# Optimization experiments

Measured on AMD Instinct MI355X. Metric: run time of the kernel, lower is better.

The kernel has to match this reference:

```python
import jax, jax.numpy as jnp
import numpy as np
from jax import lax

B, C, H, W = 32, 256, 56, 56

def _conv(x, w, stride, groups=1, pad='VALID'):
    return lax.conv_general_dilated(x, w, (stride, stride), pad,
                                    feature_group_count=groups,
                                    dimension_numbers=('NCHW', 'OIHW', 'NCHW'))

def _ln(x, g, b, eps=1e-5):
    mu = jnp.mean(x, -1, keepdims=True)
    var = jnp.mean((x - mu) ** 2, -1, keepdims=True)
    return (x - mu) * lax.rsqrt(var + eps) * g + b

def setup_inputs() -> dict:
    key = jax.random.key(0)
    ks = jax.random.split(key, 16)
    s = 0.02
    Ch = C // 2
    d = {}
    d['x'] = jax.random.normal(ks[0], (B, C, H, W), jnp.float32)
    d['Wq'] = jax.random.normal(ks[1], (C, C), jnp.float32) * s;  d['bq'] = jnp.zeros((C,), jnp.float32)
    d['Wk'] = jax.random.normal(ks[2], (C, C), jnp.float32) * s;  d['bk'] = jnp.zeros((C,), jnp.float32)
    d['Wv'] = jax.random.normal(ks[3], (C, C), jnp.float32) * s;  d['bv'] = jnp.zeros((C,), jnp.float32)
    d['sr1_w'] = jax.random.normal(ks[4], (C, C, 8, 8), jnp.float32) * s; d['sr1_b'] = jnp.zeros((C,), jnp.float32)
    d['ln1_g'] = jnp.ones((C,), jnp.float32); d['ln1_b'] = jnp.zeros((C,), jnp.float32)
    d['sr2_w'] = jax.random.normal(ks[5], (C, C, 4, 4), jnp.float32) * s; d['sr2_b'] = jnp.zeros((C,), jnp.float32)
    d['ln2_g'] = jnp.ones((C,), jnp.float32); d['ln2_b'] = jnp.zeros((C,), jnp.float32)
    d['Wkv1'] = jax.random.normal(ks[6], (C, C), jnp.float32) * s; d['bkv1'] = jnp.zeros((C,), jnp.float32)
    d['Wkv2'] = jax.random.normal(ks[7], (C, C), jnp.float32) * s; d['bkv2'] = jnp.zeros((C,), jnp.float32)
    d['lc1_w'] = jax.random.normal(ks[8], (Ch, 1, 3, 3), jnp.float32) * s; d['lc1_b'] = jnp.zeros((Ch,), jnp.float32)
    d['lc2_w'] = jax.random.normal(ks[9], (Ch, 1, 3, 3), jnp.float32) * s; d['lc2_b'] = jnp.zeros((Ch,), jnp.float32)
    d['rp_w'] = jax.random.normal(ks[10], (C, C), jnp.float32) * s;  d['rp_b'] = jnp.zeros((C,), jnp.float32)
    d['rp12_w'] = jax.random.normal(ks[11], (C, C), jnp.float32) * s; d['rp12_b'] = jnp.zeros((C,), jnp.float32)
    d['dw_w'] = jax.random.normal(ks[12], (C, 2), jnp.float32) * 0.5  # Conv3d (2,1,1) depthwise, no bias
    return d

def reference(x, Wq, bq, Wk, bk, Wv, bv, sr1_w, sr1_b, ln1_g, ln1_b,
              sr2_w, sr2_b, ln2_g, ln2_b, Wkv1, bkv1, Wkv2, bkv2,
              lc1_w, lc1_b, lc2_w, lc2_b, rp_w, rp_b, rp12_w, rp12_b, dw_w):
    Bx, Cc, h, w = x.shape
    N = h * w
    Ch = Cc // 2
    xt = x.reshape(Bx, Cc, N).transpose(0, 2, 1)                 # [B,N,C]
    q = jax.nn.softmax(xt @ Wq + bq, axis=-1)                    # softmax over channels
    q1, q2 = q[..., :Ch], q[..., Ch:]

    # spatial-reduction branches (conv -> LN -> GELU)
    x1 = _conv(x, sr1_w, 8) + sr1_b[:, None, None]               # [B,C,7,7]
    x1 = jax.nn.gelu(_ln(x1.reshape(Bx, Cc, -1).transpose(0, 2, 1), ln1_g, ln1_b), approximate=False)
    x2 = _conv(x, sr2_w, 4) + sr2_b[:, None, None]               # [B,C,14,14]
    x2 = jax.nn.gelu(_ln(x2.reshape(Bx, Cc, -1).transpose(0, 2, 1), ln2_g, ln2_b), approximate=False)

    def branch(xr, Wkv, bkv, lc_w, lc_b, qh, hh):
        kv = (xr @ Wkv + bkv).reshape(Bx, -1, 2, Ch)
        k = jax.nn.softmax(kv[:, :, 0], axis=1)                  # softmax over reduced tokens
        v = kv[:, :, 1]
        vsp = v.transpose(0, 2, 1).reshape(Bx, Ch, hh, hh)
        v = v + (_conv(vsp, lc_w, 1, groups=Ch, pad='SAME') + lc_b[:, None, None]).reshape(Bx, Ch, -1).transpose(0, 2, 1)
        ctx = jnp.einsum('bnk,bnv->bkv', k, v)                   # [B,Ch,Ch]
        return jnp.einsum('bnk,bkv->bnv', qh, ctx)               # [B,N,Ch]

    a1 = branch(x1, Wkv1, bkv1, lc1_w, lc1_b, q1, 7)
    a2 = branch(x2, Wkv2, bkv2, lc2_w, lc2_b, q2, 14)
    eff2 = jnp.concatenate([a1, a2], axis=-1)                    # [B,N,C]
    eff2 = jnp.einsum('bni,oi->bon', eff2, rp12_w).reshape(Bx, Cc, h, w) + rp12_b[None, :, None, None]

    # global efficient-attention branch
    keys = jax.nn.softmax(xt @ Wk + bk, axis=1)                  # softmax over tokens
    values = xt @ Wv + bv
    ctx = jnp.einsum('bnk,bnv->bkv', keys, values)               # [B,C,C]
    att = jnp.einsum('bnk,bkv->bnv', q, ctx)                     # [B,N,C]
    eff = jnp.einsum('bni,oi->bon', att, rp_w).reshape(Bx, Cc, h, w) + rp_b[None, :, None, None]

    # Conv3d (2,1,1) depthwise merge over the two branches
    out = eff * dw_w[:, 0][None, :, None, None] + eff2 * dw_w[:, 1][None, :, None, None]
    return out
```

## Files before the change

### kernel.cpp

```cpp
#include <hip/hip_runtime.h>
#include <hip/hip_bf16.h>
#include <math.h>

#define B_ 32
#define H_ 56
#define W_ 56
#define N_ 3136
#define NT_ 100352

typedef short short8 __attribute__((ext_vector_type(8)));
typedef float f32x4 __attribute__((ext_vector_type(4)));

__device__ __forceinline__ unsigned short f2b(float f){
  union { float f; unsigned u; } v; v.f = f;
  return (unsigned short)((v.u + 0x7FFFu + ((v.u>>16)&1u)) >> 16);
}

#define LDSW(row, bo) ((unsigned)((row)*128 + ((bo) ^ (((row)&7)<<4))))

__device__ __forceinline__ short8 ldfrag(const char* base, int row, int kk){
  return *(const short8*)(base + LDSW(row, kk*2));
}
__device__ __forceinline__ f32x4 mfma16(short8 a, short8 b, f32x4 c){
  return __builtin_amdgcn_mfma_f32_16x16x32_bf16(a, b, c, 0, 0, 0);
}

__global__ void prep_kernel(const float* __restrict__ Wq, const float* __restrict__ Wk,
                            const float* __restrict__ Wv, const float* __restrict__ Wkv1,
                            const float* __restrict__ Wkv2, const float* __restrict__ sr1w,
                            const float* __restrict__ sr2w, const float* __restrict__ rpw,
                            const float* __restrict__ rpb, const float* __restrict__ rp12w,
                            const float* __restrict__ rp12b, const float* __restrict__ dww,
                            unsigned short* WqT, unsigned short* WkT, unsigned short* WvT,
                            unsigned short* Wkv1T, unsigned short* Wkv2T,
                            unsigned short* srw1, unsigned short* srw2,
                            unsigned short* Acomb, float* bias_out)
{
  int idx = blockIdx.x*256 + threadIdx.x;
  const int total = 5*65536 + 4194304 + 1048576 + 131072 + 256;
  for (int i = idx; i < total; i += gridDim.x*256) {
    int j = i;
    if (j < 5*65536) {
      int w = j >> 16, e = j & 65535;
      int o = e >> 8, c = e & 255;
      const float* src = (w==0)?Wq:(w==1)?Wk:(w==2)?Wv:(w==3)?Wkv1:Wkv2;
      unsigned short* dst = (w==0)?WqT:(w==1)?WkT:(w==2)?WvT:(w==3)?Wkv1T:Wkv2T;
      dst[o*256+c] = f2b(src[c*256+o]);
      continue;
    }
    j -= 5*65536;
    if (j < 4194304) {
      int o = j >> 14, rem = j & 16383, pos = rem >> 8, c = rem & 255;
      srw1[j] = f2b(sr1w[o*16384 + c*64 + pos]);
      continue;
    }
    j -= 4194304;
    if (j < 1048576) {
      int o = j >> 12, rem = j & 4095, pos = rem >> 8, c = rem & 255;
      srw2[j] = f2b(sr2w[o*4096 + c*16 + pos]);
      continue;
    }
    j -= 1048576;
    if (j < 131072) {
      int o = j >> 9, i2 = j & 511;
      float v = (i2 < 256) ? dww[o*2+0]*rpw[o*256+i2]
                           : dww[o*2+1]*rp12w[o*256+(i2-256)];
      Acomb[o*512+i2] = f2b(v);
      continue;
    }
    j -= 131072;
    bias_out[j] = dww[j*2+0]*rpb[j] + dww[j*2+1]*rp12b[j];
  }
}

__global__ void transpose_kernel(const float* __restrict__ x, unsigned short* __restrict__ xt)
{
  __shared__ float tile[64][65];
  int bn = blockIdx.x; int b = bn / 49; int n0 = (bn - b*49)*64;
  int c0 = blockIdx.y*64;
  int t = threadIdx.x;
  {
    int cl = t >> 2, nq = t & 3;
    const float* src = x + ((size_t)(b*256 + c0 + cl))*N_ + n0 + nq*16;
#pragma unroll
    for (int j = 0; j < 4; j++){
      float4 v = *(const float4*)(src + j*4);
      tile[cl][nq*16 + j*4 + 0] = v.x;
      tile[cl][nq*16 + j*4 + 1] = v.y;
      tile[cl][nq*16 + j*4 + 2] = v.z;
      tile[cl][nq*16 + j*4 + 3] = v.w;
    }
  }
  __syncthreads();
  {
    int nl = t >> 2, cq = t & 3;
    unsigned short pk[16];
#pragma unroll
    for (int j=0;j<16;j++) pk[j] = f2b(tile[cq*16+j][nl]);
    unsigned short* dst = xt + ((size_t)(b*N_ + n0 + nl))*256 + c0 + cq*16;
    *(uint4*)dst = *(uint4*)&pk[0];
    *(uint4*)(dst+8) = *(uint4*)&pk[8];
  }
}

__global__ __launch_bounds__(256,2) void qkv3_kernel(
    const unsigned short* __restrict__ xt,
    const unsigned short* __restrict__ WqT, const unsigned short* __restrict__ WkT,
    const unsigned short* __restrict__ WvT,
    const float* __restrict__ bq, const float* __restrict__ bk, const float* __restrict__ bv,
    unsigned short* __restrict__ qbuf, unsigned short* __restrict__ KexpT,
    unsigned short* __restrict__ VT, float* __restrict__ s_q, float* __restrict__ s_k)
{
  __shared__ __align__(16) char smem[32768 + 32768 + 1024];
  char* At = smem;
  char* Bt = smem + 32768;
  float* redbuf = (float*)(smem + 65536);
  const int t = threadIdx.x, wave = t>>6, lane = t&63, l15 = lane&15, l4 = lane>>4;
  const int r0 = blockIdx.x*64;
  const int b = r0 / N_;
  const int nl0 = r0 - b*N_;

#pragma unroll
  for (int c4=0;c4<4;c4++)
#pragma unroll
    for (int j=0;j<2;j++){
      int chunk = j*256 + t; int row = chunk>>3, c8 = chunk&7;
      *(uint4*)(At + c4*8192 + LDSW(row, c8*16)) =
          *(const uint4*)(xt + (size_t)(r0+row)*256 + c4*64 + c8*8);
    }
  __syncthreads();

  for (int mat=0; mat<3; mat++){
    const unsigned short* BT = (mat==0)?WqT:(mat==1)?WkT:WvT;
    const float* bias = (mat==0)?bq:(mat==1)?bk:bv;
    const f32x4 vzero = {0.f,0.f,0.f,0.f};
    f32x4 acc[4][4];
#pragma unroll
    for (int i=0;i<4;i++)
#pragma unroll
      for (int j=0;j<4;j++) acc[i][j] = vzero;

    for (int k0c=0;k0c<4;k0c++){
#pragma unroll
      for (int j=0;j<8;j++){
        int chunk = j*256 + t; int row = chunk>>3, c8 = chunk&7;
        *(uint4*)(Bt + LDSW(row, c8*16)) = *(const uint4*)(BT + (size_t)row*256 + k0c*64 + c8*8);
      }
      __syncthreads();
#pragma unroll
      for (int ks=0;ks<2;ks++){
        short8 af[4], bfr[4];
#pragma unroll
        for (int mi=0;mi<4;mi++) af[mi]  = ldfrag(At + k0c*8192, mi*16 + l15, ks*32 + l4*8);
#pragma unroll
        for (int ni=0;ni<4;ni++) bfr[ni] = ldfrag(Bt, wave*64 + ni*16 + l15, ks*32 + l4*8);
#pragma unroll
        for (int mi=0;mi<4;mi++)
#pragma unroll
          for (int ni=0;ni<4;ni++)
            acc[mi][ni] = mfma16(af[mi], bfr[ni], acc[mi][ni]);
      }
      __syncthreads();
    }

    float bb4[4];
#pragma unroll
    for (int ni=0;ni<4;ni++) bb4[ni] = bias[wave*64 + ni*16 + l15];

    if (mat == 0) {
      float rs[4][4];
#pragma unroll
      for (int mi=0;mi<4;mi++)
#pragma unroll
        for (int r=0;r<4;r++) rs[mi][r] = 0.f;
#pragma unroll
      for (int mi=0;mi<4;mi++)
#pragma unroll
        for (int ni=0;ni<4;ni++)
#pragma unroll
          for (int r=0;r<4;r++){
            float e = __expf(acc[mi][ni][r] + bb4[ni]);
            acc[mi][ni][r] = e;
            rs[mi][r] += e;
          }
#pragma unroll
      for (int mi=0;mi<4;mi++)
#pragma unroll
        for (int r=0;r<4;r++){
          float s = rs[mi][r];
          s += __shfl_xor(s, 1); s += __shfl_xor(s, 2);
          s += __shfl_xor(s, 4); s += __shfl_xor(s, 8);
          rs[mi][r] = s;
        }
      if (l15 == 0){
#pragma unroll
        for (int mi=0;mi<4;mi++)
#pragma unroll
          for (int r=0;r<4;r++)
            redbuf[wave*64 + mi*16 + l4*4 + r] = rs[mi][r];
      }
      __syncthreads();
      unsigned short* qb = (unsigned short*)Bt;
#pragma unroll
      for (int mi=0;mi<4;mi++)
#pragma unroll
        for (int r=0;r<4;r++){
          int rr = mi*16 + l4*4 + r;
#pragma unroll
          for (int ni=0;ni<4;ni++)
            qb[rr*256 + wave*64 + ni*16 + l15] = f2b(acc[mi][ni][r]);
        }
      if (t < 64){
        s_q[r0 + t] = redbuf[t] + redbuf[64+t] + redbuf[128+t] + redbuf[192+t];
      }
      __syncthreads();
#pragma unroll
      for (int j=0;j<8;j++){
        int chunk = j*256 + t;
        int row = chunk >> 5, c8 = chunk & 31;
        *(uint4*)(qbuf + (size_t)(r0+row)*256 + c8*8) = *(const uint4*)(qb + row*256 + c8*8);
      }
      __syncthreads();
    } else {
      float cs[4] = {0.f,0.f,0.f,0.f};
#pragma unroll
      for (int mi=0;mi<4;mi++)
#pragma unroll
        for (int ni=0;ni<4;ni++)
#pragma unroll
          for (int r=0;r<4;r++){
            float v = acc[mi][ni][r] + bb4[ni];
            if (mat == 1){ v = __expf(v); cs[ni] += v; }
            int row = mi*16 + l4*4 + r;
            int col = wave*64 + ni*16 + l15;
            *(unsigned short*)(Bt + LDSW(col, row*2)) = f2b(v);
          }
      if (mat == 1){
#pragma unroll
        for (int ni=0;ni<4;ni++){
          float s = cs[ni];
          s += __shfl_xor(s, 16);
          s += __shfl_xor(s, 32);
          if (lane < 16) atomicAdd(&s_k[b*256 + wave*64 + ni*16 + lane], s);
        }
      }
      __syncthreads();
      unsigned short* ot = (mat==1) ? KexpT : VT;
#pragma unroll
      for (int j=0;j<8;j++){
        int chunk = j*256 + t;
        int c = chunk >> 3, n8 = chunk & 7;
        *(uint4*)(ot + ((size_t)b*256 + c)*N_ + nl0 + n8*8) = *(const uint4*)(Bt + LDSW(c, n8*16));
      }
      __syncthreads();
    }
  }
}

template<int MODE>
__global__ __launch_bounds__(256,2) void tile128_kernel(
    const unsigned short* __restrict__ Ag, const unsigned short* __restrict__ Bg,
    unsigned short* __restrict__ outg, float* __restrict__ part)
{
  __shared__ __align__(16) char smem[32768];
  char* At = smem; char* Bt = smem + 16384;
  const int b = blockIdx.x;
  const int mt = (MODE==0) ? (blockIdx.y >> 1) : blockIdx.y;
  const int nt = (MODE==0) ? (blockIdx.y & 1)  : blockIdx.z;
  const int it0 = (MODE==0) ? blockIdx.z*7 : 0;
  const int it1 = (MODE==0) ? it0+7 : 8;
  const int t = threadIdx.x;
  const int wave = t>>6, lane = t&63, l15 = lane&15, l4 = lane>>4;
  const int wm = (wave>>1)*64, wn = (wave&1)*64;
  const size_t astr = (MODE==0) ? (size_t)N_ : (size_t)512;
  const unsigned short* A  = (MODE==0) ? (Ag + ((size_t)b*256 + mt*128)*N_) : (Ag + (size_t)mt*128*512);
  const unsigned short* Bv = (MODE==0) ? (Bg + ((size_t)b*256 + nt*128)*N_) : (Bg + ((size_t)b*256 + nt*128)*512);
  const f32x4 vzero = {0.f,0.f,0.f,0.f};
  f32x4 acc[4][4];
#pragma unroll
  for (int i=0;i<4;i++)
#pragma unroll
    for (int j=0;j<4;j++) acc[i][j] = vzero;

  for (int it=it0; it<it1; it++){
    const int k0 = it*64;
#pragma unroll
    for (int j=0;j<4;j++){
      int chunk = j*256 + t; int row = chunk>>3, c8 = chunk&7;
      *(uint4*)(At + LDSW(row, c8*16)) = *(const uint4*)(A + (size_t)row*astr + k0 + c8*8);
    }
#pragma unroll
    for (int j=0;j<4;j++){
      int chunk = j*256 + t; int row = chunk>>3, c8 = chunk&7;
      *(uint4*)(Bt + LDSW(row, c8*16)) = *(const uint4*)(Bv + (size_t)row*astr + k0 + c8*8);
    }
    __syncthreads();
#pragma unroll
    for (int ks=0;ks<2;ks++){
      short8 af[4], bfr[4];
#pragma unroll
      for (int mi=0;mi<4;mi++) af[mi]  = ldfrag(At, wm + mi*16 + l15, ks*32 + l4*8);
#pragma unroll
      for (int ni=0;ni<4;ni++) bfr[ni] = ldfrag(Bt, wn + ni*16 + l15, ks*32 + l4*8);
#pragma unroll
      for (int mi=0;mi<4;mi++)
#pragma unroll
        for (int ni=0;ni<4;ni++)
          acc[mi][ni] = mfma16(af[mi], bfr[ni], acc[mi][ni]);
    }
    __syncthreads();
  }
  if (MODE==0){
    const int sk = blockIdx.z;
#pragma unroll
    for (int mi=0;mi<4;mi++)
#pragma unroll
      for (int r=0;r<4;r++){
        int kg = mt*128 + wm + mi*16 + l4*4 + r;
        size_t basep = (((size_t)sk*B_ + b)*256 + kg)*256 + nt*128 + wn;
#pragma unroll
        for (int ni=0;ni<4;ni++)
          part[basep + ni*16 + l15] = acc[mi][ni][r];
      }
  } else {
#pragma unroll
    for (int mi=0;mi<4;mi++)
#pragma unroll
      for (int r=0;r<4;r++){
        int og = mt*128 + wm + mi*16 + l4*4 + r;
#pragma unroll
        for (int ni=0;ni<4;ni++)
          outg[(size_t)b*65536 + (size_t)og*256 + nt*128 + wn + ni*16 + l15] = f2b(acc[mi][ni][r]);
      }
  }
}

__global__ __launch_bounds__(256) void ctxred_kernel(
    const float* __restrict__ part, const float* __restrict__ s_k,
    unsigned short* __restrict__ ctxcomb)
{
  int e = (blockIdx.x*256 + threadIdx.x)*4;
  int b = e >> 16; int rem = e & 65535; int kg = rem >> 8; int col = rem & 255;
  float4 s = {0.f,0.f,0.f,0.f};
#pragma unroll
  for (int sk=0; sk<7; sk++){
    float4 p = *(const float4*)(part + ((((size_t)sk*B_ + b)*256 + kg)<<8) + col);
    s.x += p.x; s.y += p.y; s.z += p.z; s.w += p.w;
  }
  float inv = 1.0f / s_k[b*256 + kg];
  unsigned short pk[4] = {f2b(s.x*inv), f2b(s.y*inv), f2b(s.z*inv), f2b(s.w*inv)};
  *(uint2*)(ctxcomb + ((size_t)b*256 + kg)*512 + col) = *(uint2*)&pk[0];
}

template<int S, int OW, int KW, int NSK, int MPB, int KTOT>
__device__ __forceinline__ void srconv_body(
    const unsigned short* __restrict__ xt, const unsigned short* __restrict__ wbf,
    float* __restrict__ part, int bid, char* At, char* Bt)
{
  const int KCH = KTOT / NSK;
  const int Mtot = B_*MPB;
  const int sk = bid % NSK, tile = bid / NSK;
  const int t = threadIdx.x, wave = t>>6, lane = t&63, l15 = lane&15, l4 = lane>>4;
  const f32x4 vzero = {0.f,0.f,0.f,0.f};
  f32x4 acc[4][4];
#pragma unroll
  for (int i=0;i<4;i++)
#pragma unroll
    for (int j=0;j<4;j++) acc[i][j] = vzero;

  size_t abase[2];
#pragma unroll
  for (int j=0;j<2;j++){
    int chunk = j*256 + t;
    int row = chunk >> 3, c8 = chunk & 7;
    int rowc = tile*64 + row; if (rowc > Mtot-1) rowc = Mtot-1;
    int b = rowc / MPB; int m = rowc - b*MPB;
    int p = m / OW; int q = m - p*OW;
    abase[j] = ((size_t)b*N_ + (size_t)(S*p)*W_ + S*q)*256 + c8*8;
  }

  for (int kt = 0; kt < KCH; kt += 64){
    const int k0 = sk*KCH + kt;
    const int pos = k0 >> 8, cc = k0 & 255;
    const int dy = pos / KW, dx = pos - dy*KW;
    const size_t off = (size_t)(dy*W_ + dx)*256 + cc;
#pragma unroll
    for (int j=0;j<2;j++){
      int chunk = j*256 + t; int row = chunk>>3, c8 = chunk&7;
      *(uint4*)(At + LDSW(row, c8*16)) = *(const uint4*)(xt + abase[j] + off);
    }
#pragma unroll
    for (int j=0;j<8;j++){
      int chunk = j*256 + t; int row = chunk>>3, c8 = chunk&7;
      *(uint4*)(Bt + LDSW(row, c8*16)) = *(const uint4*)(wbf + (size_t)row*KTOT + k0 + c8*8);
    }
    __syncthreads();
#pragma unroll
    for (int ks=0;ks<2;ks++){
      short8 af[4], bfr[4];
#pragma unroll
      for (int mi=0;mi<4;mi++) af[mi]  = ldfrag(At, mi*16 + l15, ks*32 + l4*8);
#pragma unroll
      for (int ni=0;ni<4;ni++) bfr[ni] = ldfrag(Bt, wave*64 + ni*16 + l15, ks*32 + l4*8);
#pragma unroll
      for (int mi=0;mi<4;mi++)
#pragma unroll
        for (int ni=0;ni<4;ni++)
          acc[mi][ni] = mfma16(af[mi], bfr[ni], acc[mi][ni]);
    }
    __syncthreads();
  }
#pragma unroll
  for (int mi=0;mi<4;mi++)
#pragma unroll
    for (int r=0;r<4;r++){
      int row = tile*64 + mi*16 + l4*4 + r;
      if (row < Mtot){
        size_t basep = ((size_t)sk*Mtot + row)*256;
#pragma unroll
        for (int ni=0;ni<4;ni++)
          part[basep + wave*64 + ni*16 + l15] = acc[mi][ni][r];
      }
    }
}

__global__ __launch_bounds__(256,4) void srconv_both_kernel(
    const unsigned short* __restrict__ xt, const unsigned short* __restrict__ srw1,
    const unsigned short* __restrict__ srw2, float* __restrict__ x1part,
    float* __restrict__ x2part)
{
  __shared__ __align__(16) char smem[8192 + 32768];
  if (blockIdx.x < 400)
    srconv_body<8,7,8,16,49,16384>(xt, srw1, x1part, blockIdx.x, smem, smem+8192);
  else
    srconv_body<4,14,4,4,196,4096>(xt, srw2, x2part, blockIdx.x-400, smem, smem+8192);
}

__device__ __forceinline__ void lngelu_body(
    const float* __restrict__ part, const float* __restrict__ srb,
    const float* __restrict__ g, const float* __restrict__ bb,
    unsigned short* __restrict__ out, int M, int nsk, int Mtot, int bid,
    float* red)
{
  int b = bid / M, m = bid - b*M;
  int c = threadIdx.x;
  float v = srb[c];
  for (int s=0;s<nsk;s++) v += part[((size_t)s*Mtot + b*M + m)*256 + c];
  int wave = c>>6, lane = c&63;
  float s1 = v;
  s1 += __shfl_xor(s1,1); s1 += __shfl_xor(s1,2); s1 += __shfl_xor(s1,4);
  s1 += __shfl_xor(s1,8); s1 += __shfl_xor(s1,16); s1 += __shfl_xor(s1,32);
  if (lane==0) red[wave] = s1;
  __syncthreads();
  float mu = (red[0]+red[1]+red[2]+red[3]) * (1.0f/256.0f);
  float d = v - mu;
  float s2 = d*d;
  s2 += __shfl_xor(s2,1); s2 += __shfl_xor(s2,2); s2 += __shfl_xor(s2,4);
  s2 += __shfl_xor(s2,8); s2 += __shfl_xor(s2,16); s2 += __shfl_xor(s2,32);
  if (lane==0) red[4+wave] = s2;
  __syncthreads();
  float var = (red[4]+red[5]+red[6]+red[7]) * (1.0f/256.0f);
  float y = d * rsqrtf(var + 1e-5f) * g[c] + bb[c];
  float ge = 0.5f * y * (1.0f + erff(y * 0.70710678118654752f));
  out[((size_t)b*M + m)*256 + c] = f2b(ge);
}

__global__ __launch_bounds__(256) void lngelu_both_kernel(
    const float* __restrict__ x1part, const float* __restrict__ x2part,
    const float* __restrict__ sr1b, const float* __restrict__ sr2b,
    const float* __restrict__ ln1g, const float* __restrict__ ln1b,
    const float* __restrict__ ln2g, const float* __restrict__ ln2b,
    unsigned short* __restrict__ x1g, unsigned short* __restrict__ x2g)
{
  __shared__ float red[8];
  if (blockIdx.x < 1568)
    lngelu_body(x1part, sr1b, ln1g, ln1b, x1g, 49, 16, 1568, blockIdx.x, red);
  else
    lngelu_body(x2part, sr2b, ln2g, ln2b, x2g, 196, 4, 6272, blockIdx.x-1568, red);
}

__global__ __launch_bounds__(256,2) void kv_both_kernel(
    const unsigned short* __restrict__ x1g, const unsigned short* __restrict__ Wkv1T,
    const float* __restrict__ bkv1, float* __restrict__ kexp1, float* __restrict__ vraw1,
    const unsigned short* __restrict__ x2g, const unsigned short* __restrict__ Wkv2T,
    const float* __restrict__ bkv2, float* __restrict__ kexp2, float* __restrict__ vraw2)
{
  __shared__ __align__(16) char smem[8192 + 32768];
  char* At = smem; char* Bt = smem + 8192;
  const unsigned short* A; const unsigned short* BT; const float* bias;
  float* kexp; float* vraw; int r0; int R;
  if (blockIdx.x < 25){ A=x1g; BT=Wkv1T; bias=bkv1; kexp=kexp1; vraw=vraw1; r0=blockIdx.x*64; R=1568; }
  else { A=x2g; BT=Wkv2T; bias=bkv2; kexp=kexp2; vraw=vraw2; r0=(blockIdx.x-25)*64; R=6272; }
  const int t = threadIdx.x, wave = t>>6, lane = t&63, l15 = lane&15, l4 = lane>>4;
  const f32x4 vzero = {0.f,0.f,0.f,0.f};
  f32x4 acc[4][4];
#pragma unroll
  for (int i=0;i<4;i++)
#pragma unroll
    for (int j=0;j<4;j++) acc[i][j] = vzero;

  for (int k0 = 0; k0 < 256; k0 += 64) {
#pragma unroll
    for (int j = 0; j < 2; j++){
      int chunk = j*256 + t;
      int row = chunk >> 3, c8 = chunk & 7;
      int rg = r0 + row; if (rg > R-1) rg = R-1;
      *(uint4*)(At + LDSW(row, c8*16)) = *(const uint4*)(A + (size_t)rg*256 + k0 + c8*8);
    }
#pragma unroll
    for (int j = 0; j < 8; j++){
      int chunk = j*256 + t;
      int row = chunk >> 3, c8 = chunk & 7;
      *(uint4*)(Bt + LDSW(row, c8*16)) = *(const uint4*)(BT + (size_t)row*256 + k0 + c8*8);
    }
    __syncthreads();
#pragma unroll
    for (int ks = 0; ks < 2; ks++){
      short8 af[4], bfr[4];
#pragma unroll
      for (int mi=0;mi<4;mi++) af[mi]  = ldfrag(At, mi*16 + l15, ks*32 + l4*8);
#pragma unroll
      for (int ni=0;ni<4;ni++) bfr[ni] = ldfrag(Bt, wave*64 + ni*16 + l15, ks*32 + l4*8);
#pragma unroll
      for (int mi=0;mi<4;mi++)
#pragma unroll
        for (int ni=0;ni<4;ni++)
          acc[mi][ni] = mfma16(af[mi], bfr[ni], acc[mi][ni]);
    }
    __syncthreads();
  }
  float bb4[4];
#pragma unroll
  for (int ni=0;ni<4;ni++) bb4[ni] = bias[wave*64 + ni*16 + l15];
#pragma unroll
  for (int mi=0;mi<4;mi++)
#pragma unroll
    for (int ni=0;ni<4;ni++)
#pragma unroll
      for (int r=0;r<4;r++){
        int rg = r0 + mi*16 + l4*4 + r;
        if (rg < R){
          int col = wave*64 + ni*16 + l15;
          float v = acc[mi][ni][r] + bb4[ni];
          if (col < 128) kexp[(size_t)rg*128 + col] = __expf(v);
          else           vraw[(size_t)rg*128 + (col-128)] = v;
        }
      }
}

__device__ __forceinline__ void dwconv_body(
    const float* __restrict__ vraw, const float* __restrict__ lcw,
    const float* __restrict__ lcb, float* __restrict__ vmod, int M, int OW, int idx)
{
  int ch = idx & 127; int rest = idx >> 7; int m = rest % M; int b = rest / M;
  if (b >= B_) return;
  int py = m / OW, px = m - py*OW;
  float acc = vraw[((size_t)b*M + m)*128 + ch] + lcb[ch];
#pragma unroll
  for (int dy=0;dy<3;dy++)
#pragma unroll
    for (int dx=0;dx<3;dx++){
      int yy = py+dy-1, xx = px+dx-1;
      if (yy>=0 && yy<OW && xx>=0 && xx<OW)
        acc += vraw[((size_t)b*M + yy*OW+xx)*128 + ch] * lcw[ch*9 + dy*3 + dx];
    }
  vmod[((size_t)b*M + m)*128 + ch] = acc;
}

__global__ __launch_bounds__(256) void dwconv_both_kernel(
    const float* __restrict__ vraw1, const float* __restrict__ lc1w,
    const float* __restrict__ lc1b, float* __restrict__ vmod1,
    const float* __restrict__ vraw2, const float* __restrict__ lc2w,
    const float* __restrict__ lc2b, float* __restrict__ vmod2)
{
  int gid = blockIdx.x*256 + threadIdx.x;
  if (blockIdx.x < 784) dwconv_body(vraw1, lc1w, lc1b, vmod1, 49, 7, gid);
  else dwconv_body(vraw2, lc2w, lc2b, vmod2, 196, 14, gid - 784*256);
}

__global__ __launch_bounds__(512) void ctxbr_both_kernel(
    const float* __restrict__ kexp1, const float* __restrict__ vmod1,
    const float* __restrict__ kexp2, const float* __restrict__ vmod2,
    unsigned short* __restrict__ ctxcomb)
{
  const int b = blockIdx.x;
  int kc = blockIdx.y;
  const float* kexp; const float* vmod; int M, BR;
  if (kc < 32){ kexp = kexp1; vmod = vmod1; M = 49; BR = 0; }
  else { kexp = kexp2; vmod = vmod2; M = 196; BR = 1; kc -= 32; }
  const int t = threadIdx.x;
  const int kl = t >> 7, j = t & 127;
  const int kk = kc*4 + kl;
  const float* kp = kexp + (size_t)b*M*128 + kk;
  const float* vp = vmod + (size_t)b*M*128 + j;
  float acc = 0.f, s = 0.f;
  for (int m = 0; m < M; m++){
    float kv = kp[(size_t)m*128];
    s += kv;
    acc += kv * vp[(size_t)m*128];
  }
  const int krow = BR ? (128+kk) : kk;
  unsigned short* dst = ctxcomb + ((size_t)b*256 + krow)*512;
  const int wbase = BR ? 384 : 256;
  const int zbase = BR ? 256 : 384;
  dst[wbase + j] = f2b(acc / s);
  dst[zbase + j] = 0;
}

__global__ __launch_bounds__(256,2) void final_kernel(
    const unsigned short* __restrict__ Gmat, const unsigned short* __restrict__ qbuf,
    const float* __restrict__ bias_out, const float* __restrict__ s_q,
    float* __restrict__ out)
{
  __shared__ __align__(16) char smem[16384 + 8192];
  char* At = smem; char* Bt = smem + 16384;
  const int b = blockIdx.x, ot = blockIdx.y, nt = blockIdx.z;
  const int t = threadIdx.x, wave = t>>6, lane = t&63, l15 = lane&15, l4 = lane>>4;
  const int wm = (wave>>1)*64, wn = (wave&1)*32;
  const unsigned short* A  = Gmat + ((size_t)b*256 + ot*128)*256;
  const unsigned short* Bq = qbuf + ((size_t)b*N_ + nt*64)*256;
  const f32x4 vzero = {0.f,0.f,0.f,0.f};
  f32x4 acc[4][2];
#pragma unroll
  for (int i=0;i<4;i++){ acc[i][0] = vzero; acc[i][1] = vzero; }

  for (int k0=0;k0<256;k0+=64){
#pragma unroll
    for (int j=0;j<4;j++){
      int chunk = j*256 + t; int row = chunk>>3, c8 = chunk&7;
      *(uint4*)(At + LDSW(row, c8*16)) = *(const uint4*)(A + (size_t)row*256 + k0 + c8*8);
    }
#pragma unroll
    for (int j=0;j<2;j++){
      int chunk = j*256 + t; int row = chunk>>3, c8 = chunk&7;
      *(uint4*)(Bt + LDSW(row, c8*16)) = *(const uint4*)(Bq + (size_t)row*256 + k0 + c8*8);
    }
    __syncthreads();
#pragma unroll
    for (int ks=0;ks<2;ks++){
      short8 af[4], bfr[2];
#pragma unroll
      for (int mi=0;mi<4;mi++) af[mi]  = ldfrag(At, wm + mi*16 + l15, ks*32 + l4*8);
#pragma unroll
      for (int ni=0;ni<2;ni++) bfr[ni] = ldfrag(Bt, wn + ni*16 + l15, ks*32 + l4*8);
#pragma unroll
      for (int mi=0;mi<4;mi++)
#pragma unroll
        for (int ni=0;ni<2;ni++)
          acc[mi][ni] = mfma16(af[mi], bfr[ni], acc[mi][ni]);
    }
    __syncthreads();
  }
  float iq[2];
#pragma unroll
  for (int ni=0;ni<2;ni++)
    iq[ni] = 1.0f / s_q[(size_t)b*N_ + nt*64 + wn + ni*16 + l15];
#pragma unroll
  for (int mi=0;mi<4;mi++)
#pragma unroll
    for (int r=0;r<4;r++){
      int o = ot*128 + wm + mi*16 + l4*4 + r;
      float bo = bias_out[o];
#pragma unroll
      for (int ni=0;ni<2;ni++){
        int n = nt*64 + wn + ni*16 + l15;
        out[((size_t)b*256 + o)*N_ + n] = acc[mi][ni][r]*iq[ni] + bo;
      }
    }
}

extern "C" void kernel_launch(void* const* d_in, const int* in_sizes, int n_in,
                              void* d_out, int out_size, void* d_ws, size_t ws_size,
                              hipStream_t stream)
{
  const float* x     = (const float*)d_in[0];
  const float* Wq    = (const float*)d_in[1];
  const float* bq    = (const float*)d_in[2];
  const float* Wk    = (const float*)d_in[3];
  const float* bk    = (const float*)d_in[4];
  const float* Wv    = (const float*)d_in[5];
  const float* bv    = (const float*)d_in[6];
  const float* sr1w  = (const float*)d_in[7];
  const float* sr1b  = (const float*)d_in[8];
  const float* ln1g  = (const float*)d_in[9];
  const float* ln1b  = (const float*)d_in[10];
  const float* sr2w  = (const float*)d_in[11];
  const float* sr2b  = (const float*)d_in[12];
  const float* ln2g  = (const float*)d_in[13];
  const float* ln2b  = (const float*)d_in[14];
  const float* Wkv1  = (const float*)d_in[15];
  const float* bkv1  = (const float*)d_in[16];
  const float* Wkv2  = (const float*)d_in[17];
  const float* bkv2  = (const float*)d_in[18];
  const float* lc1w  = (const float*)d_in[19];
  const float* lc1b  = (const float*)d_in[20];
  const float* lc2w  = (const float*)d_in[21];
  const float* lc2b  = (const float*)d_in[22];
  const float* rpw   = (const float*)d_in[23];
  const float* rpb   = (const float*)d_in[24];
  const float* rp12w = (const float*)d_in[25];
  const float* rp12b = (const float*)d_in[26];
  const float* dww   = (const float*)d_in[27];

  char* ws = (char*)d_ws;
  size_t off = 0;
  auto take = [&](size_t n)->char*{ char* p = ws + off; off += (n + 255) & ~(size_t)255; return p; };

  unsigned short* WqT   = (unsigned short*)take(131072);
  unsigned short* WkT   = (unsigned short*)take(131072);
  unsigned short* WvT   = (unsigned short*)take(131072);
  unsigned short* Wkv1T = (unsigned short*)take(131072);
  unsigned short* Wkv2T = (unsigned short*)take(131072);
  unsigned short* srw1  = (unsigned short*)take(8388608);
  unsigned short* srw2  = (unsigned short*)take(2097152);
  unsigned short* Acomb = (unsigned short*)take(262144);
  float* bias_out = (float*)take(1024);
  float* s_k      = (float*)take(32768);
  float* s_q      = (float*)take(401408);
  char* regionA = take(51380224);
  unsigned short* qbuf = (unsigned short*)take(51380224);
  char* regionK = take(51380224);
  char* regionV = take(51380224);
  if (off > ws_size) return;

  unsigned short* xt    = (unsigned short*)regionA;
  unsigned short* KexpT = (unsigned short*)regionK;
  float* x1part = (float*)regionK;
  float* x2part = (float*)(regionK + 25690112);
  unsigned short* VT = (unsigned short*)regionV;
  unsigned short* Gmat = (unsigned short*)regionV;
  unsigned short* x1g  = (unsigned short*)(regionV + 4194304);
  unsigned short* x2g  = (unsigned short*)(regionV + 4997120);
  float* kexp1 = (float*)(regionV + 8208384);
  float* vraw1 = (float*)(regionV + 9011200);
  float* vmod1 = (float*)(regionV + 9814016);
  float* kexp2 = (float*)(regionV + 10616832);
  float* vraw2 = (float*)(regionV + 13828096);
  float* vmod2 = (float*)(regionV + 17039360);
  unsigned short* ctxcomb = (unsigned short*)d_out;
  float* ctxpart = (float*)((char*)d_out + 8388608);

  hipMemsetAsync(s_k, 0, 32768, stream);
  prep_kernel<<<8192, 256, 0, stream>>>(Wq, Wk, Wv, Wkv1, Wkv2, sr1w, sr2w,
                                        rpw, rpb, rp12w, rp12b, dww,
                                        WqT, WkT, WvT, Wkv1T, Wkv2T, srw1, srw2,
                                        Acomb, bias_out);
  transpose_kernel<<<dim3(1568,4), 256, 0, stream>>>(x, xt);
  qkv3_kernel<<<1568, 256, 0, stream>>>(xt, WqT, WkT, WvT, bq, bk, bv,
                                        qbuf, KexpT, VT, s_q, s_k);
  tile128_kernel<0><<<dim3(32,4,7), 256, 0, stream>>>(KexpT, VT, nullptr, ctxpart);
  ctxred_kernel<<<2048, 256, 0, stream>>>(ctxpart, s_k, ctxcomb);
  srconv_both_kernel<<<792, 256, 0, stream>>>(xt, srw1, srw2, x1part, x2part);
  lngelu_both_kernel<<<7840, 256, 0, stream>>>(x1part, x2part, sr1b, sr2b,
                                               ln1g, ln1b, ln2g, ln2b, x1g, x2g);
  kv_both_kernel<<<123, 256, 0, stream>>>(x1g, Wkv1T, bkv1, kexp1, vraw1,
                                          x2g, Wkv2T, bkv2, kexp2, vraw2);
  dwconv_both_kernel<<<3920, 256, 0, stream>>>(vraw1, lc1w, lc1b, vmod1,
                                               vraw2, lc2w, lc2b, vmod2);
  ctxbr_both_kernel<<<dim3(32,64), 512, 0, stream>>>(kexp1, vmod1, kexp2, vmod2, ctxcomb);
  tile128_kernel<1><<<dim3(32,2,2), 256, 0, stream>>>(Acomb, ctxcomb, Gmat, nullptr);
  final_kernel<<<dim3(32,2,49), 256, 0, stream>>>(Gmat, qbuf, bias_out, s_q, (float*)d_out);
}
```

Baseline: 451.6 us.

## Use direct global-to-LDS loads with pre-swizzled addresses; rebalance sr-conv split-K

Replaces register-staged uint4 global loads followed by LDS stores with the global_load_lds builtin across all GEMM-style kernels. The XOR swizzle is moved onto the global source address, because the hardware writes each lane's 16 bytes to consecutive LDS slots. The aim is to save VGPRs and instructions on the load path. It also raises the split-K factor of the 8x8 strided conv from 16 to 32, reorders its block dispatch so the 4x4 branch runs first, and moves the x2part buffer into another region so the larger partial buffer fits. Risks are reliance on the LDS write pattern of the builtin (width 16 needs gfx950 support) and extra partial-sum traffic from the larger split.

Measured after the change: 424.5 us. 6.0% less time.

```diff
diff --git a/kernel.cpp b/kernel.cpp
--- a/kernel.cpp
+++ b/kernel.cpp
@@ -23,6 +23,12 @@
 }
 __device__ __forceinline__ f32x4 mfma16(short8 a, short8 b, f32x4 c){
   return __builtin_amdgcn_mfma_f32_16x16x32_bf16(a, b, c, 0, 0, 0);
+}
+
+__device__ __forceinline__ void gld16(void* lds, const void* g){
+  __builtin_amdgcn_global_load_lds((__attribute__((address_space(1))) void*)g,
+                                   (__attribute__((address_space(3))) void*)lds,
+                                   16, 0, 0);
 }
 
 __global__ void prep_kernel(const float* __restrict__ Wq, const float* __restrict__ Wk,
@@ -125,8 +131,9 @@
 #pragma unroll
     for (int j=0;j<2;j++){
       int chunk = j*256 + t; int row = chunk>>3, c8 = chunk&7;
-      *(uint4*)(At + c4*8192 + LDSW(row, c8*16)) =
-          *(const uint4*)(xt + (size_t)(r0+row)*256 + c4*64 + c8*8);
+      int c8s = c8 ^ (row&7);
+      gld16(At + c4*8192 + (j*256 + wave*64)*16,
+            xt + (size_t)(r0+row)*256 + c4*64 + c8s*8);
     }
   __syncthreads();
 
@@ -144,7 +151,8 @@
 #pragma unroll
       for (int j=0;j<8;j++){
         int chunk = j*256 + t; int row = chunk>>3, c8 = chunk&7;
-        *(uint4*)(Bt + LDSW(row, c8*16)) = *(const uint4*)(BT + (size_t)row*256 + k0c*64 + c8*8);
+        int c8s = c8 ^ (row&7);
+        gld16(Bt + (j*256 + wave*64)*16, BT + (size_t)row*256 + k0c*64 + c8s*8);
       }
       __syncthreads();
 #pragma unroll
@@ -287,12 +295,14 @@
 #pragma unroll
     for (int j=0;j<4;j++){
       int chunk = j*256 + t; int row = chunk>>3, c8 = chunk&7;
-      *(uint4*)(At + LDSW(row, c8*16)) = *(const uint4*)(A + (size_t)row*astr + k0 + c8*8);
+      int c8s = c8 ^ (row&7);
+      gld16(At + (j*256 + wave*64)*16, A + (size_t)row*astr + k0 + c8s*8);
     }
 #pragma unroll
     for (int j=0;j<4;j++){
       int chunk = j*256 + t; int row = chunk>>3, c8 = chunk&7;
-      *(uint4*)(Bt + LDSW(row, c8*16)) = *(const uint4*)(Bv + (size_t)row*astr + k0 + c8*8);
+      int c8s = c8 ^ (row&7);
+      gld16(Bt + (j*256 + wave*64)*16, Bv + (size_t)row*astr + k0 + c8s*8);
     }
     __syncthreads();
 #pragma unroll
@@ -373,10 +383,11 @@
   for (int j=0;j<2;j++){
     int chunk = j*256 + t;
     int row = chunk >> 3, c8 = chunk & 7;
+    int c8s = c8 ^ (row&7);
     int rowc = tile*64 + row; if (rowc > Mtot-1) rowc = Mtot-1;
     int b = rowc / MPB; int m = rowc - b*MPB;
     int p = m / OW; int q = m - p*OW;
-    abase[j] = ((size_t)b*N_ + (size_t)(S*p)*W_ + S*q)*256 + c8*8;
+    abase[j] = ((size_t)b*N_ + (size_t)(S*p)*W_ + S*q)*256 + c8s*8;
   }
 
   for (int kt = 0; kt < KCH; kt += 64){
@@ -386,13 +397,13 @@
     const size_t off = (size_t)(dy*W_ + dx)*256 + cc;
 #pragma unroll
     for (int j=0;j<2;j++){
-      int chunk = j*256 + t; int row = chunk>>3, c8 = chunk&7;
-      *(uint4*)(At + LDSW(row, c8*16)) = *(const uint4*)(xt + abase[j] + off);
+      gld16(At + (j*256 + wave*64)*16, xt + abase[j] + off);
     }
 #pragma unroll
     for (int j=0;j<8;j++){
       int chunk = j*256 + t; int row = chunk>>3, c8 = chunk&7;
-      *(uint4*)(Bt + LDSW(row, c8*16)) = *(const uint4*)(wbf + (size_t)row*KTOT + k0 + c8*8);
+      int c8s = c8 ^ (row&7);
+      gld16(Bt + (j*256 + wave*64)*16, wbf + (size_t)row*KTOT + k0 + c8s*8);
     }
     __syncthreads();
 #pragma unroll
@@ -430,10 +441,10 @@
     float* __restrict__ x2part)
 {
   __shared__ __align__(16) char smem[8192 + 32768];
-  if (blockIdx.x < 400)
-    srconv_body<8,7,8,16,49,16384>(xt, srw1, x1part, blockIdx.x, smem, smem+8192);
+  if (blockIdx.x < 392)
+    srconv_body<4,14,4,4,196,4096>(xt, srw2, x2part, blockIdx.x, smem, smem+8192);
   else
-    srconv_body<4,14,4,4,196,4096>(xt, srw2, x2part, blockIdx.x-400, smem, smem+8192);
+    srconv_body<8,7,8,32,49,16384>(xt, srw1, x1part, blockIdx.x-392, smem, smem+8192);
 }
 
 __device__ __forceinline__ void lngelu_body(
@@ -474,7 +485,7 @@
 {
   __shared__ float red[8];
   if (blockIdx.x < 1568)
-    lngelu_body(x1part, sr1b, ln1g, ln1b, x1g, 49, 16, 1568, blockIdx.x, red);
+    lngelu_body(x1part, sr1b, ln1g, ln1b, x1g, 49, 32, 1568, blockIdx.x, red);
   else
     lngelu_body(x2part, sr2b, ln2g, ln2b, x2g, 196, 4, 6272, blockIdx.x-1568, red);
 }
@@ -504,14 +515,16 @@
     for (int j = 0; j < 2; j++){
       int chunk = j*256 + t;
       int row = chunk >> 3, c8 = chunk & 7;
+      int c8s = c8 ^ (row&7);
       int rg = r0 + row; if (rg > R-1) rg = R-1;
-      *(uint4*)(At + LDSW(row, c8*16)) = *(const uint4*)(A + (size_t)rg*256 + k0 + c8*8);
+      gld16(At + (j*256 + wave*64)*16, A + (size_t)rg*256 + k0 + c8s*8);
     }
 #pragma unroll
     for (int j = 0; j < 8; j++){
       int chunk = j*256 + t;
       int row = chunk >> 3, c8 = chunk & 7;
-      *(uint4*)(Bt + LDSW(row, c8*16)) = *(const uint4*)(BT + (size_t)row*256 + k0 + c8*8);
+      int c8s = c8 ^ (row&7);
+      gld16(Bt + (j*256 + wave*64)*16, BT + (size_t)row*256 + k0 + c8s*8);
     }
     __syncthreads();
 #pragma unroll
@@ -628,12 +641,14 @@
 #pragma unroll
     for (int j=0;j<4;j++){
       int chunk = j*256 + t; int row = chunk>>3, c8 = chunk&7;
-      *(uint4*)(At + LDSW(row, c8*16)) = *(const uint4*)(A + (size_t)row*256 + k0 + c8*8);
+      int c8s = c8 ^ (row&7);
+      gld16(At + (j*256 + wave*64)*16, A + (size_t)row*256 + k0 + c8s*8);
     }
 #pragma unroll
     for (int j=0;j<2;j++){
       int chunk = j*256 + t; int row = chunk>>3, c8 = chunk&7;
-      *(uint4*)(Bt + LDSW(row, c8*16)) = *(const uint4*)(Bq + (size_t)row*256 + k0 + c8*8);
+      int c8s = c8 ^ (row&7);
+      gld16(Bt + (j*256 + wave*64)*16, Bq + (size_t)row*256 + k0 + c8s*8);
     }
     __syncthreads();
 #pragma unroll
@@ -726,11 +741,11 @@
   unsigned short* xt    = (unsigned short*)regionA;
   unsigned short* KexpT = (unsigned short*)regionK;
   float* x1part = (float*)regionK;
-  float* x2part = (float*)(regionK + 25690112);
   unsigned short* VT = (unsigned short*)regionV;
   unsigned short* Gmat = (unsigned short*)regionV;
   unsigned short* x1g  = (unsigned short*)(regionV + 4194304);
   unsigned short* x2g  = (unsigned short*)(regionV + 4997120);
+  float* x2part = (float*)(regionV + 8208384);
   float* kexp1 = (float*)(regionV + 8208384);
   float* vraw1 = (float*)(regionV + 9011200);
   float* vmod1 = (float*)(regionV + 9814016);
@@ -750,7 +765,7 @@
                                         qbuf, KexpT, VT, s_q, s_k);
   tile128_kernel<0><<<dim3(32,4,7), 256, 0, stream>>>(KexpT, VT, nullptr, ctxpart);
   ctxred_kernel<<<2048, 256, 0, stream>>>(ctxpart, s_k, ctxcomb);
-  srconv_both_kernel<<<792, 256, 0, stream>>>(xt, srw1, srw2, x1part, x2part);
+  srconv_both_kernel<<<1192, 256, 0, stream>>>(xt, srw1, srw2, x1part, x2part);
   lngelu_both_kernel<<<7840, 256, 0, stream>>>(x1part, x2part, sr1b, sr2b,
                                                ln1g, ln1b, ln2g, ln2b, x1g, x2g);
   kv_both_kernel<<<123, 256, 0, stream>>>(x1g, Wkv1T, bkv1, kexp1, vraw1,
```
